# Optimization experiments

Hardware: AMD Instinct MI355X
Metric: run time of the kernel (lower is better)

The kernel has to match this reference:

```python
import jax, jax.numpy as jnp
import numpy as np

NUM_HEADS = 12
HEAD_DIM = 64


def setup_inputs() -> dict:
    key = jax.random.key(0)
    ks = jax.random.split(key, 4)
    B, T, C = 2, 2048, 768
    x = jax.random.normal(ks[0], (B, T, C), dtype=jnp.float32)
    attention_mask = jnp.ones((B, 1, 1, T), dtype=jnp.int32)
    W_attn = jax.random.normal(ks[1], (C, 3 * C), dtype=jnp.float32) * 0.02
    b_attn = jnp.zeros((3 * C,), dtype=jnp.float32)
    W_proj = jax.random.normal(ks[2], (C, C), dtype=jnp.float32) * 0.02
    b_proj = jnp.zeros((C,), dtype=jnp.float32)
    return {"x": x, "attention_mask": attention_mask, "W_attn": W_attn,
            "b_attn": b_attn, "W_proj": W_proj, "b_proj": b_proj}


def reference(x, attention_mask, W_attn, b_attn, W_proj, b_proj):
    B, T, C = x.shape
    H, D = NUM_HEADS, HEAD_DIM
    # c_attn (Conv1D): y = x @ W + b -> [B, T, 3C]
    qkv = x @ W_attn + b_attn
    q, k, v = jnp.split(qkv, 3, axis=-1)
    # [B, T, C] -> [B, H, T, D]
    q = q.reshape(B, T, H, D).transpose(0, 2, 1, 3)
    k = k.reshape(B, T, H, D).transpose(0, 2, 1, 3)
    v = v.reshape(B, T, H, D).transpose(0, 2, 1, 3)
    scores = jnp.einsum('bhqd,bhkd->bhqk', q, k) / jnp.sqrt(jnp.float32(D))
    causal = jnp.tril(jnp.ones((T, T), dtype=bool))[None, None]  # [1,1,T,T]
    mask_value = jnp.finfo(scores.dtype).min
    scores = jnp.where(causal, scores, mask_value)
    scores = jnp.where(attention_mask == 0, -jnp.inf, scores)
    probs = jax.nn.softmax(scores, axis=-1)
    attn_out = jnp.einsum('bhqk,bhkd->bhqd', probs, v)
    attn_out = attn_out.transpose(0, 2, 1, 3).reshape(B, T, C)
    return attn_out @ W_proj + b_proj
```

## Files before the change

### kernel.cpp

```cpp
#include <hip/hip_runtime.h>

typedef __attribute__((ext_vector_type(8))) short bf16x8;
typedef __attribute__((ext_vector_type(4))) float f32x4;
typedef __attribute__((ext_vector_type(16))) float f32x16;

#define MFMA16(a, b, c) __builtin_amdgcn_mfma_f32_16x16x32_bf16(a, b, c, 0, 0, 0)
#define MFMA32(a, b, c) __builtin_amdgcn_mfma_f32_32x32x16_bf16(a, b, c, 0, 0, 0)
#define LOG2E 1.4426950408889634f
#define MB2 46.16624868f

#define BB 2
#define TT 2048
#define CC 768
#define HH 12
#define DD 64
#define MM (BB * TT)
#define N1 (3 * CC)
#define BH_STRIDE 131072

static __device__ __forceinline__ unsigned short f2bf(float f) {
  union { float f; unsigned u; } v; v.f = f;
  unsigned r = (v.u + 0x7FFFu + ((v.u >> 16) & 1u)) >> 16;
  return (unsigned short)r;
}

static __device__ __forceinline__ unsigned cvt_pk_bf16(float lo, float hi) {
  unsigned r;
  asm("v_cvt_pk_bf16_f32 %0, %1, %2" : "=v"(r) : "v"(lo), "v"(hi));
  return r;
}

static __device__ __forceinline__ void gload_lds16(const void* g, void* l) {
  __builtin_amdgcn_global_load_lds(
      (const __attribute__((address_space(1))) void*)g,
      (__attribute__((address_space(3))) void*)l, 16, 0, 0);
}

#define PREP_CVT 3072
#define PREP_TR1 1728
#define PREP_TR2 576
__global__ __launch_bounds__(256) void k_prep(
    const float* __restrict__ x, unsigned short* __restrict__ Xb,
    const float* __restrict__ Wa, unsigned short* __restrict__ WaT,
    const float* __restrict__ Wp, unsigned short* __restrict__ WpT,
    const int* __restrict__ mask, unsigned int* __restrict__ mb) {
  __shared__ float tile[32][33];
  const int bid = blockIdx.x;
  const int tid = threadIdx.x;
  if (bid < PREP_CVT) {
    const int i = bid * 256 + tid;
    float4 v = reinterpret_cast<const float4*>(x)[i];
    ushort4 r;
    r.x = f2bf(v.x); r.y = f2bf(v.y); r.z = f2bf(v.z); r.w = f2bf(v.w);
    reinterpret_cast<ushort4*>(Xb)[i] = r;
  } else if (bid < PREP_CVT + PREP_TR1 + PREP_TR2) {
    const bool first = bid < PREP_CVT + PREP_TR1;
    const int b = first ? bid - PREP_CVT : bid - PREP_CVT - PREP_TR1;
    const int nb = first ? 72 : 24;
    const int N = first ? N1 : CC;
    const float* W = first ? Wa : Wp;
    unsigned short* Wt = first ? WaT : WpT;
    const int n0 = (b % nb) * 32, k0 = (b / nb) * 32;
    const int tx = tid & 31, ty = tid >> 5;
#pragma unroll
    for (int i = 0; i < 4; ++i)
      tile[ty + i * 8][tx] = W[(size_t)(k0 + ty + i * 8) * N + n0 + tx];
    __syncthreads();
#pragma unroll
    for (int i = 0; i < 4; ++i)
      Wt[(size_t)(n0 + ty + i * 8) * CC + k0 + tx] = f2bf(tile[tx][ty + i * 8]);
  } else {
    if (tid < 128) {
      unsigned bits = 0;
      const int* p = mask + tid * 32;
#pragma unroll
      for (int j = 0; j < 32; ++j) bits |= (p[j] != 0 ? 1u : 0u) << j;
      mb[tid] = bits;
    }
  }
}

template <int MODE>
__global__ __launch_bounds__(256) void k_gemm(
    const unsigned short* __restrict__ A, const unsigned short* __restrict__ Bt,
    const float* __restrict__ bias, float* __restrict__ Cout, int N, int K,
    unsigned short* __restrict__ Qb, unsigned short* __restrict__ Kb,
    unsigned short* __restrict__ Vt) {
  __shared__ __align__(16) unsigned short As[3][128 * 32];
  __shared__ __align__(16) unsigned short Bs[3][128 * 32];
  const int tid = threadIdx.x;
  const int lane = tid & 63;
  const int wid = tid >> 6;
  const int l15 = lane & 15, l4 = lane >> 4;
  const int wr = wid >> 1, wc = wid & 1;
  const int brow = blockIdx.x * 128, bcol = blockIdx.y * 128;

  f32x4 acc[4][4] = {};

  const int srow = tid >> 2;
  const int usrc = (tid & 3) ^ ((tid >> 3) & 3);
  const unsigned short* gA0 = A + (size_t)(brow + srow) * K + usrc * 8;
  const unsigned short* gA1 = gA0 + (size_t)64 * K;
  const unsigned short* gB0 = Bt + (size_t)(bcol + srow) * K + usrc * 8;
  const unsigned short* gB1 = gB0 + (size_t)64 * K;
  const int dslot = tid * 8;

  const int NT = K / 32;

#define STAGE(t, buf)                                      \
  do {                                                     \
    const int ko = (t) * 32;                               \
    gload_lds16(gA0 + ko, &As[buf][dslot]);                \
    gload_lds16(gA1 + ko, &As[buf][dslot + 2048]);         \
    gload_lds16(gB0 + ko, &Bs[buf][dslot]);                \
    gload_lds16(gB1 + ko, &Bs[buf][dslot + 2048]);         \
  } while (0)

  const int swz = (l4 ^ ((l15 >> 1) & 3)) * 8;
  const int arow = wr * 64 + l15;
  const int brow2 = wc * 64 + l15;

  STAGE(0, 0);
  STAGE(1, 1);

  int cur = 0;
  for (int t = 0; t < NT - 1; ++t) {
    asm volatile("s_waitcnt vmcnt(4)" ::: "memory");
    __builtin_amdgcn_s_barrier();
    if (t + 2 < NT) {
      int nb = cur + 2; if (nb >= 3) nb -= 3;
      STAGE(t + 2, nb);
    }
    bf16x8 af[4], bfr[4];
#pragma unroll
    for (int mi = 0; mi < 4; ++mi)
      af[mi] = *reinterpret_cast<const bf16x8*>(&As[cur][(arow + mi * 16) * 32 + swz]);
#pragma unroll
    for (int ni = 0; ni < 4; ++ni)
      bfr[ni] = *reinterpret_cast<const bf16x8*>(&Bs[cur][(brow2 + ni * 16) * 32 + swz]);
    __builtin_amdgcn_s_setprio(1);
#pragma unroll
    for (int mi = 0; mi < 4; ++mi)
#pragma unroll
      for (int ni = 0; ni < 4; ++ni)
        acc[mi][ni] = MFMA16(af[mi], bfr[ni], acc[mi][ni]);
    __builtin_amdgcn_s_setprio(0);
    cur = (cur == 2) ? 0 : cur + 1;
  }
  asm volatile("s_waitcnt vmcnt(0)" ::: "memory");
  __builtin_amdgcn_s_barrier();
  {
    bf16x8 af[4], bfr[4];
#pragma unroll
    for (int mi = 0; mi < 4; ++mi)
      af[mi] = *reinterpret_cast<const bf16x8*>(&As[cur][(arow + mi * 16) * 32 + swz]);
#pragma unroll
    for (int ni = 0; ni < 4; ++ni)
      bfr[ni] = *reinterpret_cast<const bf16x8*>(&Bs[cur][(brow2 + ni * 16) * 32 + swz]);
    __builtin_amdgcn_s_setprio(1);
#pragma unroll
    for (int mi = 0; mi < 4; ++mi)
#pragma unroll
      for (int ni = 0; ni < 4; ++ni)
        acc[mi][ni] = MFMA16(af[mi], bfr[ni], acc[mi][ni]);
    __builtin_amdgcn_s_setprio(0);
  }
#undef STAGE

#pragma unroll
  for (int mi = 0; mi < 4; ++mi) {
    const int m0 = brow + wr * 64 + mi * 16 + l4 * 4;
#pragma unroll
    for (int ni = 0; ni < 4; ++ni) {
      const int n = bcol + wc * 64 + ni * 16 + l15;
      const float bv = bias[n];
      if (MODE == 0) {
#pragma unroll
        for (int r = 0; r < 4; ++r)
          Cout[(size_t)(m0 + r) * N + n] = acc[mi][ni][r] + bv;
      } else {
        const int sec = n / CC;
        const int nn = n - sec * CC;
        const int hh = nn >> 6, d = nn & 63;
        const int b = m0 >> 11;
        const int t0 = m0 & 2047;
        const size_t hbase = (size_t)(b * HH + hh) * BH_STRIDE;
        if (sec == 0) {
#pragma unroll
          for (int r = 0; r < 4; ++r) {
            const int t = t0 + r;
            Qb[hbase + ((t >> 5) * 4 + (d >> 4)) * 512 + (t & 31) * 16 + (d & 15)] =
                f2bf((acc[mi][ni][r] + bv) * 0.125f);
          }
        } else if (sec == 1) {
#pragma unroll
          for (int r = 0; r < 4; ++r) {
            const int t = t0 + r;
            Kb[hbase + ((t >> 5) * 4 + (d >> 4)) * 512 + (t & 31) * 16 + (d & 15)] =
                f2bf(acc[mi][ni][r] + bv);
          }
        } else {
          ushort4 pk;
          pk.x = f2bf(acc[mi][ni][0] + bv);
          pk.y = f2bf(acc[mi][ni][1] + bv);
          pk.z = f2bf(acc[mi][ni][2] + bv);
          pk.w = f2bf(acc[mi][ni][3] + bv);
          *reinterpret_cast<ushort4*>(
              &Vt[hbase + ((t0 >> 6) * 4 + ((t0 >> 4) & 3)) * 1024 + d * 16 + (t0 & 15)]) = pk;
        }
      }
    }
  }
}

__device__ __forceinline__ void loadk(bf16x8 (&dst)[2][4], const unsigned short* Kh,
                                      int kv0, int lo) {
  const unsigned short* kp = Kh + (kv0 >> 5) * 2048 + lo;
#pragma unroll
  for (int kg = 0; kg < 2; ++kg)
#pragma unroll
    for (int dg = 0; dg < 4; ++dg)
      dst[kg][dg] = *reinterpret_cast<const bf16x8*>(&kp[kg * 2048 + dg * 512]);
}

__device__ __forceinline__ void attn_tile(
    int kv0, const bf16x8 (&kf)[2][4], uint2 mb, const bf16x8 (&qf)[4],
    const unsigned short* __restrict__ Vh, int q0, int l31, int h, int lo,
    f32x16& o0, f32x16& o1, float& lrow) {
  const unsigned short* vp = Vh + (kv0 >> 6) * 4096 + lo;
  bf16x8 vf0[4], vf1[4];
#pragma unroll
  for (int kc = 0; kc < 4; ++kc) {
    vf0[kc] = *reinterpret_cast<const bf16x8*>(&vp[kc * 1024]);
    vf1[kc] = *reinterpret_cast<const bf16x8*>(&vp[kc * 1024 + 512]);
  }

  f32x16 s0 = {}, s1 = {};
  __builtin_amdgcn_s_setprio(1);
#pragma unroll
  for (int dg = 0; dg < 4; ++dg) s0 = MFMA32(kf[0][dg], qf[dg], s0);
#pragma unroll
  for (int dg = 0; dg < 4; ++dg) s1 = MFMA32(kf[1][dg], qf[dg], s1);
  __builtin_amdgcn_s_setprio(0);

  if ((mb.x & mb.y) != 0xffffffffu) {
#pragma unroll
    for (int r = 0; r < 16; ++r) {
      const int ki = (r & 3) + 8 * (r >> 2) + 4 * h;
      if (!((mb.x >> ki) & 1u)) s0[r] = -1e30f;
      if (!((mb.y >> ki) & 1u)) s1[r] = -1e30f;
    }
  }
  if (kv0 + 63 > q0) {
    const int q = q0 + l31;
#pragma unroll
    for (int r = 0; r < 16; ++r) {
      const int ki = kv0 + (r & 3) + 8 * (r >> 2) + 4 * h;
      if (ki > q) s0[r] = -1e30f;
      if (ki + 32 > q) s1[r] = -1e30f;
    }
  }

#pragma unroll
  for (int r = 0; r < 16; ++r) {
    s0[r] = __builtin_amdgcn_exp2f(__builtin_fmaf(s0[r], LOG2E, -MB2));
    s1[r] = __builtin_amdgcn_exp2f(__builtin_fmaf(s1[r], LOG2E, -MB2));
  }
  float ts[8];
#pragma unroll
  for (int r = 0; r < 8; ++r)
    ts[r] = (s0[2 * r] + s0[2 * r + 1]) + (s1[2 * r] + s1[2 * r + 1]);
  float ps = ((ts[0] + ts[1]) + (ts[2] + ts[3])) + ((ts[4] + ts[5]) + (ts[6] + ts[7]));
  ps += __shfl_xor(ps, 32);
  lrow += ps;

  unsigned pk0[4][2], pk1[4][2];
#pragma unroll
  for (int m = 0; m < 4; ++m)
#pragma unroll
    for (int j = 0; j < 2; ++j) {
      pk0[m][j] = cvt_pk_bf16(s0[4 * m + 2 * j], s0[4 * m + 2 * j + 1]);
      pk1[m][j] = cvt_pk_bf16(s1[4 * m + 2 * j], s1[4 * m + 2 * j + 1]);
    }

#pragma unroll
  for (int kc = 0; kc < 4; ++kc) {
    const unsigned (&pkk)[4][2] = (kc < 2) ? pk0 : pk1;
    const int c1 = (kc & 1) * 2;
    const unsigned v0 = h ? pkk[c1][0] : pkk[c1 + 1][0];
    const unsigned v1 = h ? pkk[c1][1] : pkk[c1 + 1][1];
    const unsigned r0 = (unsigned)__shfl_xor((int)v0, 32);
    const unsigned r1 = (unsigned)__shfl_xor((int)v1, 32);
    union { unsigned u[4]; bf16x8 v; } af;
    af.u[0] = h ? r0 : pkk[c1][0];
    af.u[1] = h ? r1 : pkk[c1][1];
    af.u[2] = h ? pkk[c1 + 1][0] : r0;
    af.u[3] = h ? pkk[c1 + 1][1] : r1;
    __builtin_amdgcn_s_setprio(1);
    o0 = MFMA32(af.v, vf0[kc], o0);
    o1 = MFMA32(af.v, vf1[kc], o1);
    __builtin_amdgcn_s_setprio(0);
  }
}

__global__ __launch_bounds__(64, 2) void k_attn(
    const unsigned short* __restrict__ Q, const unsigned short* __restrict__ Kb,
    const unsigned short* __restrict__ Vt, const unsigned int* __restrict__ mbits,
    float* __restrict__ pO, float* __restrict__ pL,
    unsigned short* __restrict__ AO) {
  const int lane = threadIdx.x;
  const int l31 = lane & 31;
  const int h = lane >> 5;
  const int lo = l31 * 16 + h * 8;
  const int f = blockIdx.x;
  const int xcd = f & 7;
  const int j = f >> 3;
  const int hl = j % 3;
  const int cidx = j / 3;
  const int bh = xcd * 3 + hl;
  int qb, c;
  if (cidx < 64)       { qb = 63 - (cidx >> 2); c = cidx & 3; }
  else if (cidx < 112) { const int u = cidx - 64;  qb = 47 - u / 3;    c = u % 3; }
  else if (cidx < 144) { const int u = cidx - 112; qb = 31 - (u >> 1); c = u & 1; }
  else                 { qb = 15 - (cidx - 144); c = 0; }
  int cb;
  if (qb < 16)      cb = qb;
  else if (qb < 32) cb = 16 + 2 * (qb - 16);
  else if (qb < 48) cb = 48 + 3 * (qb - 32);
  else              cb = 96 + 4 * (qb - 48);
  const int pidx = bh * 160 + cb + c;

  const int b = bh / HH;
  const int hd = bh - b * HH;
  const int q0 = qb * 32;
  const int nt = qb / 2 + 1;
  const int t0 = c * 8;
  const int t1 = (t0 + 8 < nt) ? t0 + 8 : nt;

  const unsigned short* Qh = Q + (size_t)bh * BH_STRIDE;
  const unsigned short* Kh = Kb + (size_t)bh * BH_STRIDE;
  const unsigned short* Vh = Vt + (size_t)bh * BH_STRIDE;
  const unsigned int* mbp = mbits + b * 64;

  bf16x8 qf[4];
  {
    const unsigned short* qp = Qh + (q0 >> 5) * 2048 + lo;
#pragma unroll
    for (int dg = 0; dg < 4; ++dg)
      qf[dg] = *reinterpret_cast<const bf16x8*>(&qp[dg * 512]);
  }

  f32x16 o0 = {}, o1 = {};
  float lrow = 0.f;

  bf16x8 kfA[2][4], kfB[2][4];
  uint2 mbA, mbB;
  loadk(kfA, Kh, t0 * 64, lo);
  mbA = *reinterpret_cast<const uint2*>(&mbp[t0 * 2]);

  int t = t0;
  while (true) {
    if (t + 1 < t1) {
      loadk(kfB, Kh, (t + 1) * 64, lo);
      mbB = *reinterpret_cast<const uint2*>(&mbp[(t + 1) * 2]);
    }
    attn_tile(t * 64, kfA, mbA, qf, Vh, q0, l31, h, lo, o0, o1, lrow);
    ++t; if (t >= t1) break;
    if (t + 1 < t1) {
      loadk(kfA, Kh, (t + 1) * 64, lo);
      mbA = *reinterpret_cast<const uint2*>(&mbp[(t + 1) * 2]);
    }
    attn_tile(t * 64, kfB, mbB, qf, Vh, q0, l31, h, lo, o0, o1, lrow);
    ++t; if (t >= t1) break;
  }

  if (t0 == 0 && t1 == nt) {
    const float rl = 1.0f / lrow;
#pragma unroll
    for (int r = 0; r < 16; ++r) {
      const int crow = (r & 3) + 8 * (r >> 2) + 4 * h;
      const float rb = __shfl(rl, crow);
      const size_t base = (size_t)(b * TT + q0 + crow) * CC + hd * DD;
      AO[base + l31] = f2bf(o0[r] * rb);
      AO[base + 32 + l31] = f2bf(o1[r] * rb);
    }
  } else {
    float* po = pO + (size_t)pidx * 2048;
#pragma unroll
    for (int r = 0; r < 16; ++r) {
      const int crow = (r & 3) + 8 * (r >> 2) + 4 * h;
      po[crow * 64 + l31] = o0[r];
      po[crow * 64 + 32 + l31] = o1[r];
    }
    if (lane < 32) {
      pL[pidx * 32 + lane] = lrow;
    }
  }
}

__global__ __launch_bounds__(256) void k_merge(
    const float* __restrict__ pO, const float* __restrict__ pL,
    unsigned short* __restrict__ AO) {
  const int qb = 16 + blockIdx.x, bh = blockIdx.y;
  const int b = bh / HH, hd = bh - b * HH;
  const int nt = qb / 2 + 1;
  const int nch = (nt + 7) >> 3;
  int cb;
  if (qb < 32)      cb = 16 + 2 * (qb - 16);
  else if (qb < 48) cb = 48 + 3 * (qb - 32);
  else              cb = 96 + 4 * (qb - 48);
  const int p0 = bh * 160 + cb;

  const int q = threadIdx.x >> 3;
  const int d0 = (threadIdx.x & 7) * 8;

  float lst = 0.f;
#pragma unroll
  for (int c = 0; c < 4; ++c)
    if (c < nch) lst += pL[(p0 + c) * 32 + q];
  const float inv = 1.0f / lst;

  float acc[8] = {};
#pragma unroll
  for (int c = 0; c < 4; ++c) {
    if (c < nch) {
      const float* po = pO + ((size_t)(p0 + c) * 32 + q) * 64 + d0;
      const float4 a = *reinterpret_cast<const float4*>(po);
      const float4 bq = *reinterpret_cast<const float4*>(po + 4);
      acc[0] += a.x; acc[1] += a.y; acc[2] += a.z; acc[3] += a.w;
      acc[4] += bq.x; acc[5] += bq.y; acc[6] += bq.z; acc[7] += bq.w;
    }
  }
  union { unsigned short u[8]; uint4 v; } ov;
#pragma unroll
  for (int jj = 0; jj < 8; ++jj) ov.u[jj] = f2bf(acc[jj] * inv);
  *reinterpret_cast<uint4*>(&AO[(size_t)(b * TT + qb * 32 + q) * CC + hd * DD + d0]) = ov.v;
}

extern "C" void kernel_launch(void* const* d_in, const int* in_sizes, int n_in,
                              void* d_out, int out_size, void* d_ws, size_t ws_size,
                              hipStream_t stream) {
  const float* x   = (const float*)d_in[0];
  const int* mask  = (const int*)d_in[1];
  const float* Wa  = (const float*)d_in[2];
  const float* ba  = (const float*)d_in[3];
  const float* Wp  = (const float*)d_in[4];
  const float* bp  = (const float*)d_in[5];
  float* out = (float*)d_out;

  char* ws = (char*)d_ws;
  unsigned short* Xb  = (unsigned short*)(ws);
  unsigned short* WaT = (unsigned short*)(ws + 6291456);
  unsigned short* WpT = (unsigned short*)(ws + 9830400);
  unsigned short* Qb  = (unsigned short*)(ws + 11010048);
  unsigned short* Kb  = (unsigned short*)(ws + 17301504);
  unsigned short* Vt  = (unsigned short*)(ws + 23592960);
  unsigned short* AO  = (unsigned short*)(ws + 29884416);
  unsigned int*   Mb  = (unsigned int*)(ws + 36175872);
  float*          pL  = (float*)(ws + 36667904);
  float*          pO  = (float*)(ws + 37159424);

  k_prep<<<dim3(PREP_CVT + PREP_TR1 + PREP_TR2 + 1), dim3(256), 0, stream>>>(
      x, Xb, Wa, WaT, Wp, WpT, mask, Mb);

  k_gemm<1><<<dim3(MM / 128, N1 / 128), dim3(256), 0, stream>>>(
      Xb, WaT, ba, nullptr, N1, CC, Qb, Kb, Vt);

  k_attn<<<dim3(3840), dim3(64), 0, stream>>>(Qb, Kb, Vt, Mb, pO, pL, AO);
  k_merge<<<dim3(48, BB * HH), dim3(256), 0, stream>>>(pO, pL, AO);

  k_gemm<0><<<dim3(MM / 128, CC / 128), dim3(256), 0, stream>>>(
      AO, WpT, bp, out, CC, CC, nullptr, nullptr, nullptr);
}
```

Before: 87.37 us.

## Pack four query blocks per attention workgroup and narrow output-projection GEMM tiles

After: 161.6 us. 84.9% more time.

```diff
diff --git a/kernel.cpp b/kernel.cpp
--- a/kernel.cpp
+++ b/kernel.cpp
@@ -80,69 +80,71 @@
   }
 }
 
-template <int MODE>
+template <int MODE, int BN>
 __global__ __launch_bounds__(256) void k_gemm(
     const unsigned short* __restrict__ A, const unsigned short* __restrict__ Bt,
     const float* __restrict__ bias, float* __restrict__ Cout, int N, int K,
     unsigned short* __restrict__ Qb, unsigned short* __restrict__ Kb,
     unsigned short* __restrict__ Vt) {
+  constexpr int NI = BN / 32;
   __shared__ __align__(16) unsigned short As[3][128 * 32];
-  __shared__ __align__(16) unsigned short Bs[3][128 * 32];
+  __shared__ __align__(16) unsigned short Bs[3][BN * 32];
   const int tid = threadIdx.x;
   const int lane = tid & 63;
   const int wid = tid >> 6;
   const int l15 = lane & 15, l4 = lane >> 4;
   const int wr = wid >> 1, wc = wid & 1;
-  const int brow = blockIdx.x * 128, bcol = blockIdx.y * 128;
-
-  f32x4 acc[4][4] = {};
+  const int brow = blockIdx.x * 128, bcol = blockIdx.y * BN;
+
+  f32x4 acc[4][NI] = {};
 
   const int srow = tid >> 2;
   const int usrc = (tid & 3) ^ ((tid >> 3) & 3);
   const unsigned short* gA0 = A + (size_t)(brow + srow) * K + usrc * 8;
   const unsigned short* gA1 = gA0 + (size_t)64 * K;
   const unsigned short* gB0 = Bt + (size_t)(bcol + srow) * K + usrc * 8;
-  const unsigned short* gB1 = gB0 + (size_t)64 * K;
+  const unsigned short* gB1 = (BN == 128) ? gB0 + (size_t)64 * K : gB0;
   const int dslot = tid * 8;
 
   const int NT = K / 32;
 
-#define STAGE(t, buf)                                      \
-  do {                                                     \
-    const int ko = (t) * 32;                               \
-    gload_lds16(gA0 + ko, &As[buf][dslot]);                \
-    gload_lds16(gA1 + ko, &As[buf][dslot + 2048]);         \
-    gload_lds16(gB0 + ko, &Bs[buf][dslot]);                \
-    gload_lds16(gB1 + ko, &Bs[buf][dslot + 2048]);         \
+#define STAGE(t, buf)                                       \
+  do {                                                      \
+    const int ko = (t) * 32;                                \
+    gload_lds16(gA0 + ko, &As[buf][dslot]);                 \
+    gload_lds16(gA1 + ko, &As[buf][dslot + 2048]);          \
+    gload_lds16(gB0 + ko, &Bs[buf][dslot]);                 \
+    if (BN == 128) gload_lds16(gB1 + ko, &Bs[buf][dslot + 2048]); \
   } while (0)
 
   const int swz = (l4 ^ ((l15 >> 1) & 3)) * 8;
   const int arow = wr * 64 + l15;
-  const int brow2 = wc * 64 + l15;
+  const int brow2 = wc * (BN / 2) + l15;
 
   STAGE(0, 0);
   STAGE(1, 1);
 
   int cur = 0;
   for (int t = 0; t < NT - 1; ++t) {
-    asm volatile("s_waitcnt vmcnt(4)" ::: "memory");
+    if (BN == 128) asm volatile("s_waitcnt vmcnt(4)" ::: "memory");
+    else           asm volatile("s_waitcnt vmcnt(3)" ::: "memory");
     __builtin_amdgcn_s_barrier();
     if (t + 2 < NT) {
       int nb = cur + 2; if (nb >= 3) nb -= 3;
       STAGE(t + 2, nb);
     }
-    bf16x8 af[4], bfr[4];
+    bf16x8 af[4], bfr[NI];
 #pragma unroll
     for (int mi = 0; mi < 4; ++mi)
       af[mi] = *reinterpret_cast<const bf16x8*>(&As[cur][(arow + mi * 16) * 32 + swz]);
 #pragma unroll
-    for (int ni = 0; ni < 4; ++ni)
+    for (int ni = 0; ni < NI; ++ni)
       bfr[ni] = *reinterpret_cast<const bf16x8*>(&Bs[cur][(brow2 + ni * 16) * 32 + swz]);
     __builtin_amdgcn_s_setprio(1);
 #pragma unroll
     for (int mi = 0; mi < 4; ++mi)
 #pragma unroll
-      for (int ni = 0; ni < 4; ++ni)
+      for (int ni = 0; ni < NI; ++ni)
         acc[mi][ni] = MFMA16(af[mi], bfr[ni], acc[mi][ni]);
     __builtin_amdgcn_s_setprio(0);
     cur = (cur == 2) ? 0 : cur + 1;
@@ -150,18 +152,18 @@
   asm volatile("s_waitcnt vmcnt(0)" ::: "memory");
   __builtin_amdgcn_s_barrier();
   {
-    bf16x8 af[4], bfr[4];
+    bf16x8 af[4], bfr[NI];
 #pragma unroll
     for (int mi = 0; mi < 4; ++mi)
       af[mi] = *reinterpret_cast<const bf16x8*>(&As[cur][(arow + mi * 16) * 32 + swz]);
 #pragma unroll
-    for (int ni = 0; ni < 4; ++ni)
+    for (int ni = 0; ni < NI; ++ni)
       bfr[ni] = *reinterpret_cast<const bf16x8*>(&Bs[cur][(brow2 + ni * 16) * 32 + swz]);
     __builtin_amdgcn_s_setprio(1);
 #pragma unroll
     for (int mi = 0; mi < 4; ++mi)
 #pragma unroll
-      for (int ni = 0; ni < 4; ++ni)
+      for (int ni = 0; ni < NI; ++ni)
         acc[mi][ni] = MFMA16(af[mi], bfr[ni], acc[mi][ni]);
     __builtin_amdgcn_s_setprio(0);
   }
@@ -171,8 +173,8 @@
   for (int mi = 0; mi < 4; ++mi) {
     const int m0 = brow + wr * 64 + mi * 16 + l4 * 4;
 #pragma unroll
-    for (int ni = 0; ni < 4; ++ni) {
-      const int n = bcol + wc * 64 + ni * 16 + l15;
+    for (int ni = 0; ni < NI; ++ni) {
+      const int n = bcol + wc * (BN / 2) + ni * 16 + l15;
       const float bv = bias[n];
       if (MODE == 0) {
 #pragma unroll
@@ -303,26 +305,29 @@
   }
 }
 
-__global__ __launch_bounds__(64, 2) void k_attn(
+__global__ __launch_bounds__(256, 4) void k_attn(
     const unsigned short* __restrict__ Q, const unsigned short* __restrict__ Kb,
     const unsigned short* __restrict__ Vt, const unsigned int* __restrict__ mbits,
     float* __restrict__ pO, float* __restrict__ pL,
     unsigned short* __restrict__ AO) {
-  const int lane = threadIdx.x;
+  const int tid = threadIdx.x;
+  const int lane = tid & 63;
+  const int w = tid >> 6;
   const int l31 = lane & 31;
   const int h = lane >> 5;
   const int lo = l31 * 16 + h * 8;
   const int f = blockIdx.x;
   const int xcd = f & 7;
-  const int j = f >> 3;
-  const int hl = j % 3;
-  const int cidx = j / 3;
+  const int i = f >> 3;
+  const int hl = i % 3;
+  const int j = i / 3;
   const int bh = xcd * 3 + hl;
-  int qb, c;
-  if (cidx < 64)       { qb = 63 - (cidx >> 2); c = cidx & 3; }
-  else if (cidx < 112) { const int u = cidx - 64;  qb = 47 - u / 3;    c = u % 3; }
-  else if (cidx < 144) { const int u = cidx - 112; qb = 31 - (u >> 1); c = u & 1; }
-  else                 { qb = 15 - (cidx - 144); c = 0; }
+  int g, c;
+  if (j < 16)      { g = 15 - (j >> 2); c = j & 3; }
+  else if (j < 28) { const int u = j - 16; g = 11 - u / 3; c = u % 3; }
+  else if (j < 36) { const int u = j - 28; g = 7 - (u >> 1); c = u & 1; }
+  else             { g = 3 - (j - 36); c = 0; }
+  const int qb = 4 * g + w;
   int cb;
   if (qb < 16)      cb = qb;
   else if (qb < 32) cb = 16 + 2 * (qb - 16);
@@ -463,12 +468,12 @@
   k_prep<<<dim3(PREP_CVT + PREP_TR1 + PREP_TR2 + 1), dim3(256), 0, stream>>>(
       x, Xb, Wa, WaT, Wp, WpT, mask, Mb);
 
-  k_gemm<1><<<dim3(MM / 128, N1 / 128), dim3(256), 0, stream>>>(
+  k_gemm<1, 128><<<dim3(MM / 128, N1 / 128), dim3(256), 0, stream>>>(
       Xb, WaT, ba, nullptr, N1, CC, Qb, Kb, Vt);
 
-  k_attn<<<dim3(3840), dim3(64), 0, stream>>>(Qb, Kb, Vt, Mb, pO, pL, AO);
+  k_attn<<<dim3(960), dim3(256), 0, stream>>>(Qb, Kb, Vt, Mb, pO, pL, AO);
   k_merge<<<dim3(48, BB * HH), dim3(256), 0, stream>>>(pO, pL, AO);
 
-  k_gemm<0><<<dim3(MM / 128, CC / 128), dim3(256), 0, stream>>>(
+  k_gemm<0, 64><<<dim3(MM / 128, CC / 64), dim3(256), 0, stream>>>(
       AO, WpT, bp, out, CC, CC, nullptr, nullptr, nullptr);
 }
```
